# Kernel tuning notes

Hardware: AMD Instinct MI355X
Metric: run time of the kernel (lower is better)

Reference implementation:

```python
import jax, jax.numpy as jnp
import numpy as np

H = 16
D_MODEL = 1024
D_K = D_MODEL // H
B, S = 4, 2048


def setup_inputs() -> dict:
    key = jax.random.key(0)
    ks = jax.random.split(key, 12)
    scale = 1.0 / np.sqrt(D_MODEL)
    inp = {
        "query": jax.random.normal(ks[0], (B, S, D_MODEL), jnp.float32),
        "key_in": jax.random.normal(ks[1], (B, S, D_MODEL), jnp.float32),
        "value": jax.random.normal(ks[2], (B, S, D_MODEL), jnp.float32),
        "mask": jax.random.randint(ks[3], (B, 1, S, S), 0, 2, jnp.int32),
    }
    # 4 Linear(d_model, d_model) layers: Wq, Wk, Wv, Wo (+ biases)
    names = ["q", "k", "v", "o"]
    for i, n in enumerate(names):
        inp[f"W{n}"] = jax.random.normal(ks[4 + i], (D_MODEL, D_MODEL), jnp.float32) * scale
        inp[f"b{n}"] = jax.random.normal(ks[8 + i], (D_MODEL,), jnp.float32) * scale
    return inp


def reference(query, key_in, value, mask, Wq, bq, Wk, bk, Wv, bv, Wo, bo):
    # Linear projections then split heads: [B,S,D] -> [B,H,S,Dk]
    def proj(x, W, b):
        y = jnp.einsum("bsd,ed->bse", x, W) + b  # torch Linear: x @ W.T + b
        return y.reshape(B, S, H, D_K).transpose(0, 2, 1, 3)

    q = proj(query, Wq, bq)
    k = proj(key_in, Wk, bk)
    v = proj(value, Wv, bv)

    scores = jnp.einsum("bhqd,bhkd->bhqk", q, k) / jnp.sqrt(jnp.float32(D_K))
    scores = jnp.where(mask == 0, jnp.float32(-1e9), scores)
    p_attn = jax.nn.softmax(scores, axis=-1)
    # dropout is identity in eval mode
    x = jnp.einsum("bhqk,bhkd->bhqd", p_attn, v)
    x = x.transpose(0, 2, 1, 3).reshape(B, S, D_MODEL)
    return jnp.einsum("bsd,ed->bse", x, Wo) + bo
```

## Files before the change

### kernel.cpp

```cpp
#include <hip/hip_runtime.h>
#include <hip/hip_bf16.h>

typedef __bf16 bf16_t;
typedef __attribute__((ext_vector_type(8))) __bf16 bf16x8;
typedef __attribute__((ext_vector_type(4))) __bf16 bf16x4;
typedef __attribute__((ext_vector_type(4))) float f32x4;

#define GAS __attribute__((address_space(1)))
#define LAS __attribute__((address_space(3)))

__device__ __forceinline__ void async_copy16(const bf16_t* g, bf16_t* l) {
    __builtin_amdgcn_global_load_lds((const GAS void*)g, (LAS void*)l, 16, 0, 0);
}

__global__ __launch_bounds__(256) void convert_kernel(
    const float* __restrict__ src, bf16_t* __restrict__ dst, int n)
{
    int i = (blockIdx.x * 256 + threadIdx.x) * 8;
    if (i >= n) return;
    f32x4 f0 = *(const f32x4*)(src + i);
    f32x4 f1 = *(const f32x4*)(src + i + 4);
    bf16x8 v;
#pragma unroll
    for (int j = 0; j < 4; j++) { v[j] = (bf16_t)f0[j]; v[4 + j] = (bf16_t)f1[j]; }
    *(bf16x8*)&dst[i] = v;
}

__global__ __launch_bounds__(256) void pack_mask_kernel(
    const int* __restrict__ mask, unsigned long long* __restrict__ out)
{
    int i = blockIdx.x * 256 + threadIdx.x;
    unsigned long long bits = __ballot(mask[i] != 0);
    if ((threadIdx.x & 63) == 0) out[i >> 6] = bits;
}

template<int MODE>
__global__ __launch_bounds__(256, 2) void gemm_nt(
    const bf16_t* __restrict__ A, const bf16_t* __restrict__ W,
    const float* __restrict__ bias, void* __restrict__ out_)
{
    __shared__ __align__(16) bf16_t Als[128 * 32];
    __shared__ __align__(16) bf16_t Bls[128 * 32];

    const int tid  = threadIdx.x;
    const int wave = tid >> 6, lane = tid & 63;
    const int quad = lane >> 4, lq = lane & 15;
    const int wm = wave >> 1, wn = wave & 1;
    const int tm = blockIdx.x * 128, tn = blockIdx.y * 128;
    const int K = 1024;

    const bf16_t* gA0 = A + (size_t)(tm + wave * 32 + (lane >> 2)) * K + (lane & 3) * 8;
    const bf16_t* gA1 = gA0 + (size_t)16 * K;
    const bf16_t* gB0 = W + (size_t)(tn + wave * 32 + (lane >> 2)) * K + (lane & 3) * 8;
    const bf16_t* gB1 = gB0 + (size_t)16 * K;
    bf16_t* lA0 = &Als[(wave * 32) * 32];
    bf16_t* lA1 = &Als[(wave * 32 + 16) * 32];
    bf16_t* lB0 = &Bls[(wave * 32) * 32];
    bf16_t* lB1 = &Bls[(wave * 32 + 16) * 32];

    f32x4 acc[4][4] = {};

    for (int k0 = 0; k0 < K; k0 += 32) {
        __syncthreads();
        async_copy16(gA0, lA0);
        async_copy16(gA1, lA1);
        async_copy16(gB0, lB0);
        async_copy16(gB1, lB1);
        gA0 += 32; gA1 += 32; gB0 += 32; gB1 += 32;
        __syncthreads();

        bf16x8 af[4], bfr[4];
#pragma unroll
        for (int i = 0; i < 4; i++) {
            af[i]  = *(const bf16x8*)&Als[(wm * 64 + i * 16 + lq) * 32 + quad * 8];
            bfr[i] = *(const bf16x8*)&Bls[(wn * 64 + i * 16 + lq) * 32 + quad * 8];
        }
#pragma unroll
        for (int i = 0; i < 4; i++)
#pragma unroll
            for (int j = 0; j < 4; j++) {
                if (MODE == 2)
                    acc[i][j] = __builtin_amdgcn_mfma_f32_16x16x32_bf16(bfr[j], af[i], acc[i][j], 0, 0, 0);
                else
                    acc[i][j] = __builtin_amdgcn_mfma_f32_16x16x32_bf16(af[i], bfr[j], acc[i][j], 0, 0, 0);
            }
    }

    float* outf = (float*)out_;
    bf16_t* outb = (bf16_t*)out_;
#pragma unroll
    for (int i = 0; i < 4; i++)
#pragma unroll
        for (int j = 0; j < 4; j++)
#pragma unroll
            for (int r = 0; r < 4; r++) {
                float v = acc[i][j][r];
                if (MODE == 0) {
                    int row = tm + wm * 64 + i * 16 + quad * 4 + r;
                    int col = tn + wn * 64 + j * 16 + lq;
                    outf[(size_t)row * 1024 + col] = v + bias[col];
                } else if (MODE == 1) {
                    int row = tm + wm * 64 + i * 16 + quad * 4 + r;
                    int col = tn + wn * 64 + j * 16 + lq;
                    v += bias[col];
                    int b = row >> 11, s = row & 2047;
                    int h = col >> 6,  dk = col & 63;
                    outb[(((size_t)(b * 16 + h) * 2048 + s) << 6) + dk] = (bf16_t)v;
                } else {
                    int n = tn + wn * 64 + j * 16 + quad * 4 + r;
                    int m = tm + wm * 64 + i * 16 + lq;
                    v += bias[n];
                    int b = m >> 11, s = m & 2047;
                    int h = n >> 6,  dk = n & 63;
                    outb[((size_t)((b * 16 + h) * 64 + dk) << 11) + s] = (bf16_t)v;
                }
            }
}

#define LDK 72
#define LDV 40
#define LDP 40

__global__ __launch_bounds__(256, 2) void attn_kernel(
    const bf16_t* __restrict__ Q, const bf16_t* __restrict__ Kh,
    const bf16_t* __restrict__ Vt, const unsigned int* __restrict__ mp,
    bf16_t* __restrict__ X)
{
    __shared__ __align__(16) bf16_t Kls[32 * LDK];
    __shared__ __align__(16) bf16_t Vls[64 * LDV];
    __shared__ __align__(16) bf16_t Pls[4][16 * LDP];

    const int tid  = threadIdx.x;
    const int wave = tid >> 6, lane = tid & 63;
    const int quad = lane >> 4, lq = lane & 15;
    const int bh = blockIdx.y;
    const int b  = bh >> 4;
    const int qw = blockIdx.x * 64 + wave * 16;

    const bf16_t* qptr = Q + ((size_t)bh * 2048 + qw + lq) * 64 + quad * 8;
    bf16x8 qf0 = *(const bf16x8*)qptr;
    bf16x8 qf1 = *(const bf16x8*)(qptr + 32);

    f32x4 o[4] = {};
    float lsum = 0.f;

    const int kr = tid >> 3, kc = tid & 7;
    const int vr = tid >> 2, vc = tid & 3;
    const bf16_t* gK = Kh + ((size_t)bh * 2048 + kr) * 64 + kc * 8;
    const bf16_t* gV = Vt + ((size_t)bh * 64 + vr) * 2048 + vc * 8;

    const unsigned int* mrow = mp + ((size_t)(b << 11) + qw + lq) * 64;

    for (int kt = 0; kt < 64; kt++) {
        unsigned int w = mrow[kt];
        bf16x8 kstage = *(const bf16x8*)gK;
        bf16x8 vstage = *(const bf16x8*)gV;
        gK += 2048; gV += 32;

        __syncthreads();
        *(bf16x8*)&Kls[kr * LDK + kc * 8] = kstage;
        *(bf16x8*)&Vls[vr * LDV + vc * 8] = vstage;
        __syncthreads();

        bf16_t* pb = &Pls[wave][0];
        const unsigned int wq = w >> (quad * 4);
#pragma unroll
        for (int nt = 0; nt < 2; nt++) {
            const bf16_t* krow = &Kls[(nt * 16 + lq) * LDK];
            bf16x8 kf0 = *(const bf16x8*)(krow + quad * 8);
            bf16x8 kf1 = *(const bf16x8*)(krow + 32 + quad * 8);
            f32x4 z = {};
            z = __builtin_amdgcn_mfma_f32_16x16x32_bf16(kf0, qf0, z, 0, 0, 0);
            z = __builtin_amdgcn_mfma_f32_16x16x32_bf16(kf1, qf1, z, 0, 0, 0);
            bf16x4 pk;
#pragma unroll
            for (int r = 0; r < 4; r++) {
                float sv = ((wq >> (nt * 16 + r)) & 1) ? z[r] * 0.125f : -1e9f;
                float p = __expf(sv);
                lsum += p;
                pk[r] = (bf16_t)p;
            }
            *(bf16x4*)&pb[lq * LDP + nt * 16 + quad * 4] = pk;
        }

        bf16x8 pf = *(const bf16x8*)&pb[lq * LDP + quad * 8];
#pragma unroll
        for (int dt = 0; dt < 4; dt++) {
            bf16x8 vf = *(const bf16x8*)&Vls[(dt * 16 + lq) * LDV + quad * 8];
            o[dt] = __builtin_amdgcn_mfma_f32_16x16x32_bf16(pf, vf, o[dt], 0, 0, 0);
        }
    }

    lsum += __shfl_xor(lsum, 16);
    lsum += __shfl_xor(lsum, 32);
    float rl[4];
#pragma unroll
    for (int r = 0; r < 4; r++) {
        float lv = __shfl(lsum, quad * 4 + r);
        rl[r] = (lv > 0.f) ? 1.0f / lv : 0.f;
    }
    const int h = bh & 15;
#pragma unroll
    for (int dt = 0; dt < 4; dt++)
#pragma unroll
        for (int r = 0; r < 4; r++) {
            int qrow = qw + quad * 4 + r;
            X[((size_t)(b * 2048) + qrow) * 1024 + h * 64 + dt * 16 + lq] =
                (bf16_t)(o[dt][r] * rl[r]);
        }
}

extern "C" void kernel_launch(void* const* d_in, const int* in_sizes, int n_in,
                              void* d_out, int out_size, void* d_ws, size_t ws_size,
                              hipStream_t stream)
{
    const float* query  = (const float*)d_in[0];
    const float* key_in = (const float*)d_in[1];
    const float* value  = (const float*)d_in[2];
    const int*   mask   = (const int*)d_in[3];

    char* ws = (char*)d_ws;
    const size_t SZ  = (size_t)8192 * 1024 * 2;
    const size_t MPK = (size_t)2 * 1024 * 1024;
    const size_t WSZ = (size_t)1024 * 1024 * 2;
    bf16_t* C   = (bf16_t*)(ws);
    bf16_t* Qb  = (bf16_t*)(ws + SZ);
    bf16_t* Kb  = (bf16_t*)(ws + 2 * SZ);
    bf16_t* Vtb = (bf16_t*)(ws + 3 * SZ);
    unsigned long long* mpack = (unsigned long long*)(ws + 4 * SZ);
    bf16_t* Wc[4];
    for (int i = 0; i < 4; i++)
        Wc[i] = (bf16_t*)(ws + 4 * SZ + MPK + i * WSZ);

    const size_t NEED = 4 * SZ + MPK + 4 * WSZ;
    if (ws_size < NEED) return;

    const int NACT = 8192 * 1024;
    for (int i = 0; i < 4; i++)
        convert_kernel<<<512, 256, 0, stream>>>((const float*)d_in[4 + 2 * i],
                                                Wc[i], 1024 * 1024);
    pack_mask_kernel<<<65536, 256, 0, stream>>>(mask, mpack);

    dim3 gg(64, 8);
    convert_kernel<<<4096, 256, 0, stream>>>(query, C, NACT);
    gemm_nt<1><<<gg, 256, 0, stream>>>(C, Wc[0], (const float*)d_in[5], Qb);
    convert_kernel<<<4096, 256, 0, stream>>>(key_in, C, NACT);
    gemm_nt<1><<<gg, 256, 0, stream>>>(C, Wc[1], (const float*)d_in[7], Kb);
    convert_kernel<<<4096, 256, 0, stream>>>(value, C, NACT);
    gemm_nt<2><<<gg, 256, 0, stream>>>(C, Wc[2], (const float*)d_in[9], Vtb);

    attn_kernel<<<dim3(32, 64), 256, 0, stream>>>(Qb, Kb, Vtb,
                                                  (const unsigned int*)mpack, C);
    gemm_nt<0><<<gg, 256, 0, stream>>>(C, Wc[3], (const float*)d_in[11], d_out);
}
```

Baseline: 473.0 us.

## Enlarge attention tiles to 32 query rows per wave and 64-key steps

Each wave now processes 32 query rows against 64-key tiles, with the block covering 128 queries, so each K/V tile staged in LDS serves twice as many MFMAs and the loop needs half as many barrier pairs. The next K/V tile's global loads are issued right after the barrier to overlap with compute. The 1/sqrt(dk) scale is folded into the Q projection epilogue, removing a multiply per score. The bigger tiles raise LDS use and register pressure, and the block count is halved.

```diff
diff --git a/kernel.cpp b/kernel.cpp
--- a/kernel.cpp
+++ b/kernel.cpp
@@ -37,7 +37,7 @@
 template<int MODE>
 __global__ __launch_bounds__(256, 2) void gemm_nt(
     const bf16_t* __restrict__ A, const bf16_t* __restrict__ W,
-    const float* __restrict__ bias, void* __restrict__ out_)
+    const float* __restrict__ bias, void* __restrict__ out_, float oscale)
 {
     __shared__ __align__(16) bf16_t Als[128 * 32];
     __shared__ __align__(16) bf16_t Bls[128 * 32];
@@ -98,18 +98,18 @@
                 if (MODE == 0) {
                     int row = tm + wm * 64 + i * 16 + quad * 4 + r;
                     int col = tn + wn * 64 + j * 16 + lq;
-                    outf[(size_t)row * 1024 + col] = v + bias[col];
+                    outf[(size_t)row * 1024 + col] = (v + bias[col]) * oscale;
                 } else if (MODE == 1) {
                     int row = tm + wm * 64 + i * 16 + quad * 4 + r;
                     int col = tn + wn * 64 + j * 16 + lq;
-                    v += bias[col];
+                    v = (v + bias[col]) * oscale;
                     int b = row >> 11, s = row & 2047;
                     int h = col >> 6,  dk = col & 63;
                     outb[(((size_t)(b * 16 + h) * 2048 + s) << 6) + dk] = (bf16_t)v;
                 } else {
                     int n = tn + wn * 64 + j * 16 + quad * 4 + r;
                     int m = tm + wm * 64 + i * 16 + lq;
-                    v += bias[n];
+                    v = (v + bias[n]) * oscale;
                     int b = m >> 11, s = m & 2047;
                     int h = n >> 6,  dk = n & 63;
                     outb[((size_t)((b * 16 + h) * 64 + dk) << 11) + s] = (bf16_t)v;
@@ -118,96 +118,122 @@
 }
 
 #define LDK 72
-#define LDV 40
-#define LDP 40
-
-__global__ __launch_bounds__(256, 2) void attn_kernel(
+#define LDV 72
+#define LDP 72
+
+__global__ __launch_bounds__(256, 4) void attn_kernel(
     const bf16_t* __restrict__ Q, const bf16_t* __restrict__ Kh,
     const bf16_t* __restrict__ Vt, const unsigned int* __restrict__ mp,
     bf16_t* __restrict__ X)
 {
-    __shared__ __align__(16) bf16_t Kls[32 * LDK];
+    __shared__ __align__(16) bf16_t Kls[64 * LDK];
     __shared__ __align__(16) bf16_t Vls[64 * LDV];
-    __shared__ __align__(16) bf16_t Pls[4][16 * LDP];
+    __shared__ __align__(16) bf16_t Pls[4][32 * LDP];
 
     const int tid  = threadIdx.x;
     const int wave = tid >> 6, lane = tid & 63;
     const int quad = lane >> 4, lq = lane & 15;
     const int bh = blockIdx.y;
-    const int b  = bh >> 4;
-    const int qw = blockIdx.x * 64 + wave * 16;
-
-    const bf16_t* qptr = Q + ((size_t)bh * 2048 + qw + lq) * 64 + quad * 8;
-    bf16x8 qf0 = *(const bf16x8*)qptr;
-    bf16x8 qf1 = *(const bf16x8*)(qptr + 32);
-
-    f32x4 o[4] = {};
-    float lsum = 0.f;
-
-    const int kr = tid >> 3, kc = tid & 7;
-    const int vr = tid >> 2, vc = tid & 3;
-    const bf16_t* gK = Kh + ((size_t)bh * 2048 + kr) * 64 + kc * 8;
-    const bf16_t* gV = Vt + ((size_t)bh * 64 + vr) * 2048 + vc * 8;
-
-    const unsigned int* mrow = mp + ((size_t)(b << 11) + qw + lq) * 64;
-
-    for (int kt = 0; kt < 64; kt++) {
-        unsigned int w = mrow[kt];
-        bf16x8 kstage = *(const bf16x8*)gK;
-        bf16x8 vstage = *(const bf16x8*)gV;
-        gK += 2048; gV += 32;
-
-        __syncthreads();
-        *(bf16x8*)&Kls[kr * LDK + kc * 8] = kstage;
-        *(bf16x8*)&Vls[vr * LDV + vc * 8] = vstage;
-        __syncthreads();
+    const int b  = bh >> 4, h = bh & 15;
+    const int qwv = blockIdx.x * 128 + wave * 32;
+
+    bf16x8 qf[2][2];
+#pragma unroll
+    for (int qs = 0; qs < 2; qs++) {
+        const bf16_t* qptr = Q + ((size_t)bh * 2048 + qwv + qs * 16 + lq) * 64 + quad * 8;
+        qf[qs][0] = *(const bf16x8*)qptr;
+        qf[qs][1] = *(const bf16x8*)(qptr + 32);
+    }
+
+    f32x4 o[2][4] = {};
+    f32x4 ls[2] = {};
+
+    const int sr = tid >> 3, sc = tid & 7;
+    const bf16_t* gK0 = Kh + ((size_t)bh * 2048 + sr) * 64 + sc * 8;
+    const bf16_t* gK1 = gK0 + 32 * 64;
+    const bf16_t* gV0 = Vt + ((size_t)bh * 64 + sr) * 2048 + sc * 8;
+    const bf16_t* gV1 = gV0 + 32 * 2048;
+    bf16_t* lK0 = &Kls[sr * LDK + sc * 8];
+    bf16_t* lK1 = &Kls[(sr + 32) * LDK + sc * 8];
+    bf16_t* lV0 = &Vls[sr * LDV + sc * 8];
+    bf16_t* lV1 = &Vls[(sr + 32) * LDV + sc * 8];
+
+    const unsigned int* mr0 = mp + ((size_t)(b << 11) + qwv + lq) * 64;
+
+    bf16x8 ks0 = *(const bf16x8*)gK0, ks1 = *(const bf16x8*)gK1;
+    bf16x8 vs0 = *(const bf16x8*)gV0, vs1 = *(const bf16x8*)gV1;
+
+    for (int kt = 0; kt < 32; kt++) {
+        __syncthreads();
+        *(bf16x8*)lK0 = ks0; *(bf16x8*)lK1 = ks1;
+        *(bf16x8*)lV0 = vs0; *(bf16x8*)lV1 = vs1;
+        __syncthreads();
+        if (kt < 31) {
+            gK0 += 4096; gK1 += 4096; gV0 += 64; gV1 += 64;
+            ks0 = *(const bf16x8*)gK0; ks1 = *(const bf16x8*)gK1;
+            vs0 = *(const bf16x8*)gV0; vs1 = *(const bf16x8*)gV1;
+        }
+        unsigned int w[2][2];
+        w[0][0] = mr0[2 * kt];        w[0][1] = mr0[2 * kt + 1];
+        w[1][0] = mr0[2 * kt + 1024]; w[1][1] = mr0[2 * kt + 1025];
 
         bf16_t* pb = &Pls[wave][0];
-        const unsigned int wq = w >> (quad * 4);
-#pragma unroll
-        for (int nt = 0; nt < 2; nt++) {
+#pragma unroll
+        for (int nt = 0; nt < 4; nt++) {
             const bf16_t* krow = &Kls[(nt * 16 + lq) * LDK];
             bf16x8 kf0 = *(const bf16x8*)(krow + quad * 8);
             bf16x8 kf1 = *(const bf16x8*)(krow + 32 + quad * 8);
-            f32x4 z = {};
-            z = __builtin_amdgcn_mfma_f32_16x16x32_bf16(kf0, qf0, z, 0, 0, 0);
-            z = __builtin_amdgcn_mfma_f32_16x16x32_bf16(kf1, qf1, z, 0, 0, 0);
-            bf16x4 pk;
+#pragma unroll
+            for (int qs = 0; qs < 2; qs++) {
+                f32x4 z = {};
+                z = __builtin_amdgcn_mfma_f32_16x16x32_bf16(kf0, qf[qs][0], z, 0, 0, 0);
+                z = __builtin_amdgcn_mfma_f32_16x16x32_bf16(kf1, qf[qs][1], z, 0, 0, 0);
+                unsigned int wq = w[qs][nt >> 1] >> ((nt & 1) * 16 + quad * 4);
+                bf16x4 pk;
+#pragma unroll
+                for (int r = 0; r < 4; r++) {
+                    float sv = ((wq >> r) & 1) ? z[r] : -1e9f;
+                    float p = __expf(sv);
+                    ls[qs][r] += p;
+                    pk[r] = (bf16_t)p;
+                }
+                *(bf16x4*)&pb[(qs * 16 + lq) * LDP + nt * 16 + quad * 4] = pk;
+            }
+        }
+
+#pragma unroll
+        for (int c = 0; c < 2; c++) {
+            bf16x8 pf0 = *(const bf16x8*)&pb[lq * LDP + c * 32 + quad * 8];
+            bf16x8 pf1 = *(const bf16x8*)&pb[(16 + lq) * LDP + c * 32 + quad * 8];
+#pragma unroll
+            for (int dt = 0; dt < 4; dt++) {
+                bf16x8 vf = *(const bf16x8*)&Vls[(dt * 16 + lq) * LDV + c * 32 + quad * 8];
+                o[0][dt] = __builtin_amdgcn_mfma_f32_16x16x32_bf16(pf0, vf, o[0][dt], 0, 0, 0);
+                o[1][dt] = __builtin_amdgcn_mfma_f32_16x16x32_bf16(pf1, vf, o[1][dt], 0, 0, 0);
+            }
+        }
+    }
+
+#pragma unroll
+    for (int qs = 0; qs < 2; qs++) {
+        float l = (ls[qs][0] + ls[qs][1]) + (ls[qs][2] + ls[qs][3]);
+        l += __shfl_xor(l, 16);
+        l += __shfl_xor(l, 32);
+        float rl[4];
+#pragma unroll
+        for (int r = 0; r < 4; r++) {
+            float lv = __shfl(l, quad * 4 + r);
+            rl[r] = (lv > 0.f) ? 1.0f / lv : 0.f;
+        }
+#pragma unroll
+        for (int dt = 0; dt < 4; dt++)
 #pragma unroll
             for (int r = 0; r < 4; r++) {
-                float sv = ((wq >> (nt * 16 + r)) & 1) ? z[r] * 0.125f : -1e9f;
-                float p = __expf(sv);
-                lsum += p;
-                pk[r] = (bf16_t)p;
-            }
-            *(bf16x4*)&pb[lq * LDP + nt * 16 + quad * 4] = pk;
-        }
-
-        bf16x8 pf = *(const bf16x8*)&pb[lq * LDP + quad * 8];
-#pragma unroll
-        for (int dt = 0; dt < 4; dt++) {
-            bf16x8 vf = *(const bf16x8*)&Vls[(dt * 16 + lq) * LDV + quad * 8];
-            o[dt] = __builtin_amdgcn_mfma_f32_16x16x32_bf16(pf, vf, o[dt], 0, 0, 0);
-        }
-    }
-
-    lsum += __shfl_xor(lsum, 16);
-    lsum += __shfl_xor(lsum, 32);
-    float rl[4];
-#pragma unroll
-    for (int r = 0; r < 4; r++) {
-        float lv = __shfl(lsum, quad * 4 + r);
-        rl[r] = (lv > 0.f) ? 1.0f / lv : 0.f;
-    }
-    const int h = bh & 15;
-#pragma unroll
-    for (int dt = 0; dt < 4; dt++)
-#pragma unroll
-        for (int r = 0; r < 4; r++) {
-            int qrow = qw + quad * 4 + r;
-            X[((size_t)(b * 2048) + qrow) * 1024 + h * 64 + dt * 16 + lq] =
-                (bf16_t)(o[dt][r] * rl[r]);
-        }
+                int qrow = qwv + qs * 16 + quad * 4 + r;
+                X[((size_t)(b * 2048) + qrow) * 1024 + h * 64 + dt * 16 + lq] =
+                    (bf16_t)(o[qs][dt][r] * rl[r]);
+            }
+    }
 }
 
 extern "C" void kernel_launch(void* const* d_in, const int* in_sizes, int n_in,
@@ -243,13 +269,13 @@
 
     dim3 gg(64, 8);
     convert_kernel<<<4096, 256, 0, stream>>>(query, C, NACT);
-    gemm_nt<1><<<gg, 256, 0, stream>>>(C, Wc[0], (const float*)d_in[5], Qb);
+    gemm_nt<1><<<gg, 256, 0, stream>>>(C, Wc[0], (const float*)d_in[5], Qb, 0.125f);
     convert_kernel<<<4096, 256, 0, stream>>>(key_in, C, NACT);
-    gemm_nt<1><<<gg, 256, 0, stream>>>(C, Wc[1], (const float*)d_in[7], Kb);
+    gemm_nt<1><<<gg, 256, 0, stream>>>(C, Wc[1], (const float*)d_in[7], Kb, 1.0f);
     convert_kernel<<<4096, 256, 0, stream>>>(value, C, NACT);
-    gemm_nt<2><<<gg, 256, 0, stream>>>(C, Wc[2], (const float*)d_in[9], Vtb);
-
-    attn_kernel<<<dim3(32, 64), 256, 0, stream>>>(Qb, Kb, Vtb,
+    gemm_nt<2><<<gg, 256, 0, stream>>>(C, Wc[2], (const float*)d_in[9], Vtb, 1.0f);
+
+    attn_kernel<<<dim3(16, 64), 256, 0, stream>>>(Qb, Kb, Vtb,
                                                   (const unsigned int*)mpack, C);
-    gemm_nt<0><<<gg, 256, 0, stream>>>(C, Wc[3], (const float*)d_in[11], d_out);
-}
+    gemm_nt<0><<<gg, 256, 0, stream>>>(C, Wc[3], (const float*)d_in[11], d_out, 1.0f);
+}
```

New measurement: 443.0 us. 1.07x faster.
